# Performance work log

Hardware: AMD Instinct MI355X
Metric: run time of the kernel (lower is better)

The kernel has to match this reference:

```python
import jax, jax.numpy as jnp
import numpy as np

B, S, E, H = 4, 2048, 1024, 16
D = E // H  # head_size = 64

def setup_inputs() -> dict:
    key = jax.random.key(0)
    k1, k2, k3 = jax.random.split(key, 3)
    x = jax.random.normal(k1, (B, S, E), dtype=jnp.float32)
    # torch Linear weight is (out,in); we store transposed (in,out) for x @ W
    w_attn = jax.random.normal(k2, (E, 3 * E), dtype=jnp.float32) * (1.0 / np.sqrt(E))
    w_proj = jax.random.normal(k3, (E, E), dtype=jnp.float32) * (1.0 / np.sqrt(E))
    return {"x": x, "w_attn": w_attn, "w_proj": w_proj}

def reference(x, w_attn, w_proj):
    b, s, e = x.shape
    qkv = x @ w_attn                      # (B,S,3E)
    q, k, v = jnp.split(qkv, 3, axis=2)
    # (B,S,H,D) -> (B,H,S,D)
    q = q.reshape(b, s, H, D).transpose(0, 2, 1, 3)
    k = k.reshape(b, s, H, D).transpose(0, 2, 1, 3)
    v = v.reshape(b, s, H, D).transpose(0, 2, 1, 3)
    scale = 1.0 / np.sqrt(D).astype(np.float32)
    att = jnp.einsum('bhqd,bhkd->bhqk', q, k) * scale  # (B,H,S,S)
    causal = jnp.tril(jnp.ones((s, s), dtype=bool))
    att = jnp.where(causal[None, None, :, :], att, jnp.float32(-jnp.inf))
    att = jax.nn.softmax(att, axis=-1)
    # dropout layers are identity in eval mode
    y = jnp.einsum('bhqk,bhkd->bhqd', att, v)          # (B,H,S,D)
    y = y.transpose(0, 2, 1, 3).reshape(b, s, e)       # (B,S,E)
    return y @ w_proj
```

## Files before the change

kernel.cpp:

```cpp
#include <hip/hip_runtime.h>
#include <hip/hip_bf16.h>
#include <cstdint>

typedef __attribute__((ext_vector_type(8))) short bf16x8;
typedef __attribute__((ext_vector_type(4))) short short4v;
typedef __attribute__((ext_vector_type(4))) float f32x4;

#define MFMA(a, b, c) __builtin_amdgcn_mfma_f32_16x16x32_bf16((a), (b), (c), 0, 0, 0)

__device__ __forceinline__ unsigned short f2bf(float f) {
  union { float f; unsigned int u; } v;
  v.f = f;
  unsigned int r = v.u + 0x7FFFu + ((v.u >> 16) & 1u);
  return (unsigned short)(r >> 16);
}

__device__ __forceinline__ unsigned short f2bf_ru(float f) {
  union { float f; unsigned int u; } v;
  v.f = f;
  return (unsigned short)((v.u + 0x8000u) >> 16);
}

__device__ __forceinline__ void async_cp16(const unsigned short* g, unsigned short* l) {
  __builtin_amdgcn_global_load_lds(
      (const __attribute__((address_space(1))) unsigned int*)g,
      (__attribute__((address_space(3))) unsigned int*)l, 16, 0, 0);
}

__global__ __launch_bounds__(256) void cvt_x(const float* __restrict__ in,
                                             unsigned short* __restrict__ out) {
  size_t i = ((size_t)blockIdx.x * 256 + threadIdx.x) * 8;
  float4 a = *(const float4*)(in + i);
  float4 b = *(const float4*)(in + i + 4);
  bf16x8 p;
  p[0] = (short)f2bf(a.x); p[1] = (short)f2bf(a.y);
  p[2] = (short)f2bf(a.z); p[3] = (short)f2bf(a.w);
  p[4] = (short)f2bf(b.x); p[5] = (short)f2bf(b.y);
  p[6] = (short)f2bf(b.z); p[7] = (short)f2bf(b.w);
  *(bf16x8*)(out + i) = p;
}

__global__ __launch_bounds__(256) void transpose_cvt(const float* __restrict__ in,
                                                     unsigned short* __restrict__ out,
                                                     int K, int N) {
  __shared__ float tile[64][65];
  int k0 = blockIdx.x * 64;
  int n0 = blockIdx.y * 64;
  int c = threadIdx.x & 63;
  int rb = threadIdx.x >> 6;
#pragma unroll
  for (int i = 0; i < 16; ++i) {
    int r = rb * 16 + i;
    tile[r][c] = in[(size_t)(k0 + r) * N + (n0 + c)];
  }
  __syncthreads();
#pragma unroll
  for (int i = 0; i < 16; ++i) {
    int r = rb * 16 + i;
    out[(size_t)(n0 + r) * K + (k0 + c)] = f2bf(tile[c][r]);
  }
}

__global__ __launch_bounds__(256) void gemm_qkv(const unsigned short* __restrict__ X,
                                                const unsigned short* __restrict__ WT,
                                                unsigned short* __restrict__ qb,
                                                unsigned short* __restrict__ kb,
                                                unsigned short* __restrict__ vt) {
  const int K = 1024;
  __shared__ unsigned short As[128 * 64];
  __shared__ unsigned short Bs[128 * 64];
  int t = threadIdx.x, lane = t & 63, w = t >> 6;
  int quad = lane >> 4, l15 = lane & 15;
  int sl7 = l15 & 7;
  int wm = (w >> 1) * 64, wn = (w & 1) * 64;
  int row0 = blockIdx.y * 128, col0 = blockIdx.x * 128;
  int srow = w * 8 + (lane >> 3);
  int schunk = (lane & 7) ^ (lane >> 3);
  const unsigned short* aSrc = X + (size_t)(row0 + srow) * K + schunk * 8;
  const unsigned short* bSrc = WT + (size_t)(col0 + srow) * K + schunk * 8;
  unsigned short* ldsA = &As[(w * 8) * 64];
  unsigned short* ldsB = &Bs[(w * 8) * 64];
  f32x4 zero4 = {0.f, 0.f, 0.f, 0.f};
  f32x4 acc[4][4];
#pragma unroll
  for (int i = 0; i < 4; ++i)
#pragma unroll
    for (int j = 0; j < 4; ++j) acc[i][j] = zero4;

  for (int k0 = 0; k0 < K; k0 += 64) {
    __syncthreads();
#pragma unroll
    for (int i = 0; i < 4; ++i)
      async_cp16(aSrc + (size_t)i * 32 * K + k0, ldsA + i * 32 * 64);
#pragma unroll
    for (int i = 0; i < 4; ++i)
      async_cp16(bSrc + (size_t)i * 32 * K + k0, ldsB + i * 32 * 64);
    __syncthreads();
#pragma unroll
    for (int h = 0; h < 2; ++h) {
      bf16x8 af[4], bfr[4];
#pragma unroll
      for (int mt = 0; mt < 4; ++mt)
        af[mt] = *(const bf16x8*)&As[(wm + mt * 16 + l15) * 64 +
                                     ((h * 4 + quad) ^ sl7) * 8];
#pragma unroll
      for (int nt = 0; nt < 4; ++nt)
        bfr[nt] = *(const bf16x8*)&Bs[(wn + nt * 16 + l15) * 64 +
                                      ((h * 4 + quad) ^ sl7) * 8];
#pragma unroll
      for (int mt = 0; mt < 4; ++mt)
#pragma unroll
        for (int nt = 0; nt < 4; ++nt)
          acc[mt][nt] = MFMA(af[mt], bfr[nt], acc[mt][nt]);
    }
  }

  const float qscale = 0.125f * 1.4426950408889634f;
#pragma unroll
  for (int mt = 0; mt < 4; ++mt) {
    int rix0 = row0 + wm + mt * 16 + quad * 4;
    int b = rix0 >> 11;
    int s0 = rix0 & 2047;
#pragma unroll
    for (int nt = 0; nt < 4; ++nt) {
      int c = col0 + wn + nt * 16 + l15;
      int which = c >> 10;
      int e = c & 1023;
      int h = e >> 6, d = e & 63;
      size_t bh = (size_t)b * 16 + h;
      if (which == 2) {
        short4v pv;
#pragma unroll
        for (int r = 0; r < 4; ++r) pv[r] = (short)f2bf(acc[mt][nt][r]);
        *(short4v*)(vt + (bh * 64 + d) * 2048 + s0) = pv;
      } else {
        unsigned short* dst = (which == 0) ? qb : kb;
        float sc = (which == 0) ? qscale : 1.0f;
#pragma unroll
        for (int r = 0; r < 4; ++r)
          dst[(bh * 2048 + (s0 + r)) * 64 + d] = f2bf(acc[mt][nt][r] * sc);
      }
    }
  }
}

__global__ __launch_bounds__(256) void flash_attn(const unsigned short* __restrict__ qb,
                                                  const unsigned short* __restrict__ kb,
                                                  const unsigned short* __restrict__ vt,
                                                  unsigned short* __restrict__ yb) {
  __shared__ unsigned short Ks[64 * 68];
  __shared__ unsigned short Vs[64 * 68];
  __shared__ unsigned short P[4][16 * 68];
  int idx = blockIdx.x;
  int qt = 31 - (idx >> 6);
  int bh = idx & 63;
  int t = threadIdx.x, lane = t & 63, w = t >> 6;
  int quad = lane >> 4, l15 = lane & 15;
  int qrow0 = qt * 64 + w * 16;

  const unsigned short* Qp = qb + ((size_t)bh * 2048 + qrow0 + l15) * 64 + quad * 8;
  bf16x8 aq0 = *(const bf16x8*)Qp;
  bf16x8 aq1 = *(const bf16x8*)(Qp + 32);
  f32x4 zero4 = {0.f, 0.f, 0.f, 0.f};
  f32x4 o[4], accl;
  accl = zero4;
#pragma unroll
  for (int nt = 0; nt < 4; ++nt) o[nt] = zero4;
  bf16x8 ones;
#pragma unroll
  for (int i = 0; i < 8; ++i) ones[i] = (short)0x3F80;
  unsigned short* Pw = P[w];

  int srow = t >> 2;
  int sseg = (t & 3) * 8;
  const unsigned short* Kg = kb + ((size_t)bh * 2048 + srow) * 64 + sseg;
  const unsigned short* Vg = vt + ((size_t)bh * 64 + srow) * 2048 + sseg;
  int ktmax = qt;

  bf16x8 kg0 = *(const bf16x8*)Kg;
  bf16x8 kg1 = *(const bf16x8*)(Kg + 32);
  bf16x8 vg0 = *(const bf16x8*)Vg;
  bf16x8 vg1 = *(const bf16x8*)(Vg + 32);

  for (int kt = 0; kt <= ktmax; ++kt) {
    int kbase = kt * 64;
    __syncthreads();
    *(bf16x8*)&Ks[srow * 68 + sseg] = kg0;
    *(bf16x8*)&Ks[srow * 68 + sseg + 32] = kg1;
    *(bf16x8*)&Vs[srow * 68 + sseg] = vg0;
    *(bf16x8*)&Vs[srow * 68 + sseg + 32] = vg1;
    __syncthreads();
    if (kt < ktmax) {
      const unsigned short* nk = Kg + (size_t)(kbase + 64) * 64;
      kg0 = *(const bf16x8*)nk;
      kg1 = *(const bf16x8*)(nk + 32);
      const unsigned short* nv = Vg + kbase + 64;
      vg0 = *(const bf16x8*)nv;
      vg1 = *(const bf16x8*)(nv + 32);
    }
    if (kbase > qrow0 + 15) continue;

    bf16x8 kf0[4], kf1[4], vf0[4], vf1[4];
#pragma unroll
    for (int nt = 0; nt < 4; ++nt) {
      kf0[nt] = *(const bf16x8*)&Ks[(nt * 16 + l15) * 68 + quad * 8];
      kf1[nt] = *(const bf16x8*)&Ks[(nt * 16 + l15) * 68 + 32 + quad * 8];
      vf0[nt] = *(const bf16x8*)&Vs[(nt * 16 + l15) * 68 + quad * 8];
      vf1[nt] = *(const bf16x8*)&Vs[(nt * 16 + l15) * 68 + 32 + quad * 8];
    }

    f32x4 sv[4];
#pragma unroll
    for (int nt = 0; nt < 4; ++nt) {
      f32x4 z = zero4;
      z = MFMA(aq0, kf0[nt], z);
      z = MFMA(aq1, kf1[nt], z);
      sv[nt] = z;
    }
    if (kbase + 63 > qrow0) {
#pragma unroll
      for (int nt = 0; nt < 4; ++nt) {
        int col = kbase + nt * 16 + l15;
#pragma unroll
        for (int r = 0; r < 4; ++r)
          if (col > qrow0 + quad * 4 + r) sv[nt][r] = -1e30f;
      }
    }
#pragma unroll
    for (int nt = 0; nt < 4; ++nt)
#pragma unroll
      for (int r = 0; r < 4; ++r) {
        float p = __builtin_amdgcn_exp2f(sv[nt][r]);
        Pw[(quad * 4 + r) * 68 + nt * 16 + l15] = f2bf_ru(p);
      }
    bf16x8 ap0 = *(const bf16x8*)&Pw[l15 * 68 + quad * 8];
    bf16x8 ap1 = *(const bf16x8*)&Pw[l15 * 68 + 32 + quad * 8];
    accl = MFMA(ap0, ones, accl);
    accl = MFMA(ap1, ones, accl);
#pragma unroll
    for (int nt = 0; nt < 4; ++nt) {
      o[nt] = MFMA(ap0, vf0[nt], o[nt]);
      o[nt] = MFMA(ap1, vf1[nt], o[nt]);
    }
  }

  int b = bh >> 4, h = bh & 15;
  float inv[4];
#pragma unroll
  for (int r = 0; r < 4; ++r) inv[r] = 1.0f / accl[r];
#pragma unroll
  for (int nt = 0; nt < 4; ++nt) {
    int e = h * 64 + nt * 16 + l15;
#pragma unroll
    for (int r = 0; r < 4; ++r) {
      int srow_g = qrow0 + quad * 4 + r;
      yb[((size_t)b * 2048 + srow_g) * 1024 + e] = f2bf(o[nt][r] * inv[r]);
    }
  }
}

__global__ __launch_bounds__(256) void gemm_proj(const unsigned short* __restrict__ Y,
                                                 const unsigned short* __restrict__ WT,
                                                 float* __restrict__ out) {
  const int K = 1024;
  __shared__ unsigned short As[128 * 64];
  __shared__ unsigned short Bs[128 * 64];
  int t = threadIdx.x, lane = t & 63, w = t >> 6;
  int quad = lane >> 4, l15 = lane & 15;
  int sl7 = l15 & 7;
  int wm = (w >> 1) * 64, wn = (w & 1) * 64;
  int row0 = blockIdx.y * 128, col0 = blockIdx.x * 128;
  int srow = w * 8 + (lane >> 3);
  int schunk = (lane & 7) ^ (lane >> 3);
  const unsigned short* aSrc = Y + (size_t)(row0 + srow) * K + schunk * 8;
  const unsigned short* bSrc = WT + (size_t)(col0 + srow) * K + schunk * 8;
  unsigned short* ldsA = &As[(w * 8) * 64];
  unsigned short* ldsB = &Bs[(w * 8) * 64];
  f32x4 zero4 = {0.f, 0.f, 0.f, 0.f};
  f32x4 acc[4][4];
#pragma unroll
  for (int i = 0; i < 4; ++i)
#pragma unroll
    for (int j = 0; j < 4; ++j) acc[i][j] = zero4;

  for (int k0 = 0; k0 < K; k0 += 64) {
    __syncthreads();
#pragma unroll
    for (int i = 0; i < 4; ++i)
      async_cp16(aSrc + (size_t)i * 32 * K + k0, ldsA + i * 32 * 64);
#pragma unroll
    for (int i = 0; i < 4; ++i)
      async_cp16(bSrc + (size_t)i * 32 * K + k0, ldsB + i * 32 * 64);
    __syncthreads();
#pragma unroll
    for (int h = 0; h < 2; ++h) {
      bf16x8 af[4], bfr[4];
#pragma unroll
      for (int mt = 0; mt < 4; ++mt)
        af[mt] = *(const bf16x8*)&As[(wm + mt * 16 + l15) * 64 +
                                     ((h * 4 + quad) ^ sl7) * 8];
#pragma unroll
      for (int nt = 0; nt < 4; ++nt)
        bfr[nt] = *(const bf16x8*)&Bs[(wn + nt * 16 + l15) * 64 +
                                      ((h * 4 + quad) ^ sl7) * 8];
#pragma unroll
      for (int mt = 0; mt < 4; ++mt)
#pragma unroll
        for (int nt = 0; nt < 4; ++nt)
          acc[mt][nt] = MFMA(af[mt], bfr[nt], acc[mt][nt]);
    }
  }

#pragma unroll
  for (int mt = 0; mt < 4; ++mt) {
    int rix0 = row0 + wm + mt * 16 + quad * 4;
#pragma unroll
    for (int nt = 0; nt < 4; ++nt) {
      int c = col0 + wn + nt * 16 + l15;
#pragma unroll
      for (int r = 0; r < 4; ++r)
        out[(size_t)(rix0 + r) * 1024 + c] = acc[mt][nt][r];
    }
  }
}

extern "C" void kernel_launch(void* const* d_in, const int* in_sizes, int n_in,
                              void* d_out, int out_size, void* d_ws, size_t ws_size,
                              hipStream_t stream) {
  const float* x = (const float*)d_in[0];
  const float* w_attn = (const float*)d_in[1];
  const float* w_proj = (const float*)d_in[2];
  float* out = (float*)d_out;
  char* ws = (char*)d_ws;
  unsigned short* wT  = (unsigned short*)(ws + 0);
  unsigned short* wpT = (unsigned short*)(ws + 6291456);
  unsigned short* qb  = (unsigned short*)(ws + 8388608);
  unsigned short* kb  = (unsigned short*)(ws + 25165824);
  unsigned short* vt  = (unsigned short*)(ws + 41943040);
  unsigned short* xyb = (unsigned short*)(ws + 58720256);

  cvt_x<<<4096, 256, 0, stream>>>(x, xyb);
  transpose_cvt<<<dim3(16, 48), 256, 0, stream>>>(w_attn, wT, 1024, 3072);
  transpose_cvt<<<dim3(16, 16), 256, 0, stream>>>(w_proj, wpT, 1024, 1024);
  gemm_qkv<<<dim3(24, 64), 256, 0, stream>>>(xyb, wT, qb, kb, vt);
  flash_attn<<<dim3(2048), 256, 0, stream>>>(qb, kb, vt, xyb);
  gemm_proj<<<dim3(8, 64), 256, 0, stream>>>(xyb, wpT, out);
}
```

Baseline: 281.3 us.

## Enlarge flash-attention query tiles, pair causal tiles per block, read V directly

Each block now handles two 128-row query tiles, paired as (15-p, p) so every block does about the same amount of causal work. Each wave owns 32 query rows, split into two 16-row sub-tiles, and reuses every K tile it loads from shared memory. V is no longer staged in LDS and is read directly from global memory into registers. The grid drops from 2048 to 512 blocks with launch_bounds(256,2). This cuts K staging traffic and barriers per query row and balances the causal workload, at the cost of uncoalesced, unprefetched V global loads, higher register pressure and fewer blocks in flight.

```diff
diff --git a/kernel.cpp b/kernel.cpp
--- a/kernel.cpp
+++ b/kernel.cpp
@@ -144,117 +144,134 @@
   }
 }
 
-__global__ __launch_bounds__(256) void flash_attn(const unsigned short* __restrict__ qb,
-                                                  const unsigned short* __restrict__ kb,
-                                                  const unsigned short* __restrict__ vt,
-                                                  unsigned short* __restrict__ yb) {
+__global__ __launch_bounds__(256, 2) void flash_attn(const unsigned short* __restrict__ qb,
+                                                     const unsigned short* __restrict__ kb,
+                                                     const unsigned short* __restrict__ vt,
+                                                     unsigned short* __restrict__ yb) {
   __shared__ unsigned short Ks[64 * 68];
-  __shared__ unsigned short Vs[64 * 68];
   __shared__ unsigned short P[4][16 * 68];
   int idx = blockIdx.x;
-  int qt = 31 - (idx >> 6);
   int bh = idx & 63;
+  int p = idx >> 6;
   int t = threadIdx.x, lane = t & 63, w = t >> 6;
   int quad = lane >> 4, l15 = lane & 15;
-  int qrow0 = qt * 64 + w * 16;
-
-  const unsigned short* Qp = qb + ((size_t)bh * 2048 + qrow0 + l15) * 64 + quad * 8;
-  bf16x8 aq0 = *(const bf16x8*)Qp;
-  bf16x8 aq1 = *(const bf16x8*)(Qp + 32);
+  unsigned short* Pw = P[w];
   f32x4 zero4 = {0.f, 0.f, 0.f, 0.f};
-  f32x4 o[4], accl;
-  accl = zero4;
-#pragma unroll
-  for (int nt = 0; nt < 4; ++nt) o[nt] = zero4;
   bf16x8 ones;
 #pragma unroll
   for (int i = 0; i < 8; ++i) ones[i] = (short)0x3F80;
-  unsigned short* Pw = P[w];
 
   int srow = t >> 2;
   int sseg = (t & 3) * 8;
   const unsigned short* Kg = kb + ((size_t)bh * 2048 + srow) * 64 + sseg;
-  const unsigned short* Vg = vt + ((size_t)bh * 64 + srow) * 2048 + sseg;
-  int ktmax = qt;
-
-  bf16x8 kg0 = *(const bf16x8*)Kg;
-  bf16x8 kg1 = *(const bf16x8*)(Kg + 32);
-  bf16x8 vg0 = *(const bf16x8*)Vg;
-  bf16x8 vg1 = *(const bf16x8*)(Vg + 32);
-
-  for (int kt = 0; kt <= ktmax; ++kt) {
-    int kbase = kt * 64;
-    __syncthreads();
-    *(bf16x8*)&Ks[srow * 68 + sseg] = kg0;
-    *(bf16x8*)&Ks[srow * 68 + sseg + 32] = kg1;
-    *(bf16x8*)&Vs[srow * 68 + sseg] = vg0;
-    *(bf16x8*)&Vs[srow * 68 + sseg + 32] = vg1;
-    __syncthreads();
-    if (kt < ktmax) {
-      const unsigned short* nk = Kg + (size_t)(kbase + 64) * 64;
-      kg0 = *(const bf16x8*)nk;
-      kg1 = *(const bf16x8*)(nk + 32);
-      const unsigned short* nv = Vg + kbase + 64;
-      vg0 = *(const bf16x8*)nv;
-      vg1 = *(const bf16x8*)(nv + 32);
-    }
-    if (kbase > qrow0 + 15) continue;
-
-    bf16x8 kf0[4], kf1[4], vf0[4], vf1[4];
-#pragma unroll
-    for (int nt = 0; nt < 4; ++nt) {
-      kf0[nt] = *(const bf16x8*)&Ks[(nt * 16 + l15) * 68 + quad * 8];
-      kf1[nt] = *(const bf16x8*)&Ks[(nt * 16 + l15) * 68 + 32 + quad * 8];
-      vf0[nt] = *(const bf16x8*)&Vs[(nt * 16 + l15) * 68 + quad * 8];
-      vf1[nt] = *(const bf16x8*)&Vs[(nt * 16 + l15) * 68 + 32 + quad * 8];
-    }
-
-    f32x4 sv[4];
-#pragma unroll
-    for (int nt = 0; nt < 4; ++nt) {
-      f32x4 z = zero4;
-      z = MFMA(aq0, kf0[nt], z);
-      z = MFMA(aq1, kf1[nt], z);
-      sv[nt] = z;
-    }
-    if (kbase + 63 > qrow0) {
+  int b = bh >> 4, h = bh & 15;
+
+  for (int seg = 0; seg < 2; ++seg) {
+    int qt = seg ? p : (15 - p);
+    int qrow0 = qt * 128 + w * 32;
+    int ktmax = 2 * qt + 1;
+
+    bf16x8 aq0[2], aq1[2];
+#pragma unroll
+    for (int s = 0; s < 2; ++s) {
+      const unsigned short* Qp =
+          qb + ((size_t)bh * 2048 + qrow0 + s * 16 + l15) * 64 + quad * 8;
+      aq0[s] = *(const bf16x8*)Qp;
+      aq1[s] = *(const bf16x8*)(Qp + 32);
+    }
+    f32x4 o[2][4], accl[2];
+#pragma unroll
+    for (int s = 0; s < 2; ++s) {
+      accl[s] = zero4;
+#pragma unroll
+      for (int nt = 0; nt < 4; ++nt) o[s][nt] = zero4;
+    }
+
+    bf16x8 kg0 = *(const bf16x8*)Kg;
+    bf16x8 kg1 = *(const bf16x8*)(Kg + 32);
+
+    for (int kt = 0; kt <= ktmax; ++kt) {
+      int kbase = kt * 64;
+      __syncthreads();
+      *(bf16x8*)&Ks[srow * 68 + sseg] = kg0;
+      *(bf16x8*)&Ks[srow * 68 + sseg + 32] = kg1;
+      __syncthreads();
+      if (kt < ktmax) {
+        const unsigned short* nk = Kg + (size_t)(kbase + 64) * 64;
+        kg0 = *(const bf16x8*)nk;
+        kg1 = *(const bf16x8*)(nk + 32);
+      }
+      if (kbase > qrow0 + 31) continue;
+
+      bf16x8 vf0[4], vf1[4];
 #pragma unroll
       for (int nt = 0; nt < 4; ++nt) {
-        int col = kbase + nt * 16 + l15;
-#pragma unroll
-        for (int r = 0; r < 4; ++r)
-          if (col > qrow0 + quad * 4 + r) sv[nt][r] = -1e30f;
-      }
-    }
-#pragma unroll
-    for (int nt = 0; nt < 4; ++nt)
-#pragma unroll
-      for (int r = 0; r < 4; ++r) {
-        float p = __builtin_amdgcn_exp2f(sv[nt][r]);
-        Pw[(quad * 4 + r) * 68 + nt * 16 + l15] = f2bf_ru(p);
-      }
-    bf16x8 ap0 = *(const bf16x8*)&Pw[l15 * 68 + quad * 8];
-    bf16x8 ap1 = *(const bf16x8*)&Pw[l15 * 68 + 32 + quad * 8];
-    accl = MFMA(ap0, ones, accl);
-    accl = MFMA(ap1, ones, accl);
-#pragma unroll
-    for (int nt = 0; nt < 4; ++nt) {
-      o[nt] = MFMA(ap0, vf0[nt], o[nt]);
-      o[nt] = MFMA(ap1, vf1[nt], o[nt]);
-    }
-  }
-
-  int b = bh >> 4, h = bh & 15;
-  float inv[4];
-#pragma unroll
-  for (int r = 0; r < 4; ++r) inv[r] = 1.0f / accl[r];
-#pragma unroll
-  for (int nt = 0; nt < 4; ++nt) {
-    int e = h * 64 + nt * 16 + l15;
-#pragma unroll
-    for (int r = 0; r < 4; ++r) {
-      int srow_g = qrow0 + quad * 4 + r;
-      yb[((size_t)b * 2048 + srow_g) * 1024 + e] = f2bf(o[nt][r] * inv[r]);
+        const unsigned short* Vp =
+            vt + ((size_t)bh * 64 + nt * 16 + l15) * 2048 + kbase + quad * 8;
+        vf0[nt] = *(const bf16x8*)Vp;
+        vf1[nt] = *(const bf16x8*)(Vp + 32);
+      }
+      bf16x8 kf0[4], kf1[4];
+#pragma unroll
+      for (int nt = 0; nt < 4; ++nt) {
+        kf0[nt] = *(const bf16x8*)&Ks[(nt * 16 + l15) * 68 + quad * 8];
+        kf1[nt] = *(const bf16x8*)&Ks[(nt * 16 + l15) * 68 + 32 + quad * 8];
+      }
+
+#pragma unroll
+      for (int s = 0; s < 2; ++s) {
+        int rowb = qrow0 + s * 16;
+        if (kbase > rowb + 15) continue;
+        f32x4 sv[4];
+#pragma unroll
+        for (int nt = 0; nt < 4; ++nt) {
+          f32x4 z = zero4;
+          z = MFMA(aq0[s], kf0[nt], z);
+          z = MFMA(aq1[s], kf1[nt], z);
+          sv[nt] = z;
+        }
+        if (kbase + 63 > rowb) {
+#pragma unroll
+          for (int nt = 0; nt < 4; ++nt) {
+            int col = kbase + nt * 16 + l15;
+#pragma unroll
+            for (int r = 0; r < 4; ++r)
+              if (col > rowb + quad * 4 + r) sv[nt][r] = -1e30f;
+          }
+        }
+#pragma unroll
+        for (int nt = 0; nt < 4; ++nt)
+#pragma unroll
+          for (int r = 0; r < 4; ++r) {
+            float pv = __builtin_amdgcn_exp2f(sv[nt][r]);
+            Pw[(quad * 4 + r) * 68 + nt * 16 + l15] = f2bf_ru(pv);
+          }
+        bf16x8 ap0 = *(const bf16x8*)&Pw[l15 * 68 + quad * 8];
+        bf16x8 ap1 = *(const bf16x8*)&Pw[l15 * 68 + 32 + quad * 8];
+        accl[s] = MFMA(ap0, ones, accl[s]);
+        accl[s] = MFMA(ap1, ones, accl[s]);
+#pragma unroll
+        for (int nt = 0; nt < 4; ++nt) {
+          o[s][nt] = MFMA(ap0, vf0[nt], o[s][nt]);
+          o[s][nt] = MFMA(ap1, vf1[nt], o[s][nt]);
+        }
+      }
+    }
+
+#pragma unroll
+    for (int s = 0; s < 2; ++s) {
+      float inv[4];
+#pragma unroll
+      for (int r = 0; r < 4; ++r) inv[r] = 1.0f / accl[s][r];
+#pragma unroll
+      for (int nt = 0; nt < 4; ++nt) {
+        int e = h * 64 + nt * 16 + l15;
+#pragma unroll
+        for (int r = 0; r < 4; ++r) {
+          int srow_g = qrow0 + s * 16 + quad * 4 + r;
+          yb[((size_t)b * 2048 + srow_g) * 1024 + e] = f2bf(o[s][nt][r] * inv[r]);
+        }
+      }
     }
   }
 }
@@ -343,6 +360,6 @@
   transpose_cvt<<<dim3(16, 48), 256, 0, stream>>>(w_attn, wT, 1024, 3072);
   transpose_cvt<<<dim3(16, 16), 256, 0, stream>>>(w_proj, wpT, 1024, 1024);
   gemm_qkv<<<dim3(24, 64), 256, 0, stream>>>(xyb, wT, qb, kb, vt);
-  flash_attn<<<dim3(2048), 256, 0, stream>>>(qb, kb, vt, xyb);
+  flash_attn<<<dim3(512), 256, 0, stream>>>(qb, kb, vt, xyb);
   gemm_proj<<<dim3(8, 64), 256, 0, stream>>>(xyb, wpT, out);
 }
```

After: 262.2 us. -6.8%, faster.
